# Optimization experiments

Measured on AMD Instinct MI355X. Metric: run time of the kernel, lower is better.

Reference implementation:

```python
import jax, jax.numpy as jnp
import numpy as np

D_MODEL = 1024
NUM_HEADS = 16
D_K = D_MODEL // NUM_HEADS
B, S = 2, 2048


def setup_inputs() -> dict:
    key = jax.random.key(0)
    ks = jax.random.split(key, 11)
    lim = 1.0 / np.sqrt(D_MODEL)  # torch Linear default init range
    def lin(kw, kb):
        W = jax.random.uniform(kw, (D_MODEL, D_MODEL), jnp.float32, -lim, lim)
        b = jax.random.uniform(kb, (D_MODEL,), jnp.float32, -lim, lim)
        return W, b
    Wq, bq = lin(ks[0], ks[1])
    Wk, bk = lin(ks[2], ks[3])
    Wv, bv = lin(ks[4], ks[5])
    Wo, bo = lin(ks[6], ks[7])
    return {
        "Q": jax.random.normal(ks[8], (B, S, D_MODEL), jnp.float32),
        "K": jax.random.normal(ks[9], (B, S, D_MODEL), jnp.float32),
        "V": jax.random.normal(ks[10], (B, S, D_MODEL), jnp.float32),
        "Wq": Wq, "bq": bq, "Wk": Wk, "bk": bk,
        "Wv": Wv, "bv": bv, "Wo": Wo, "bo": bo,
        "validate": False,
    }


def _split_heads(x):
    b, s, _ = x.shape
    return x.reshape(b, s, NUM_HEADS, D_K).transpose(0, 2, 1, 3)  # [B,H,S,Dk]


def reference(Q, K, V, Wq, bq, Wk, bk, Wv, bv, Wo, bo, validate):
    # Linear projections (torch Linear: x @ W.T + b)
    q = _split_heads(Q @ Wq.T + bq)
    k = _split_heads(K @ Wk.T + bk)
    v = _split_heads(V @ Wv.T + bv)
    scale = 1.0 / jnp.sqrt(jnp.asarray(D_K, q.dtype))
    scores = jnp.einsum("bhqd,bhkd->bhqk", q, k) * scale  # [B,H,S,S]
    attn = jax.nn.softmax(scores, axis=-1)
    out = jnp.einsum("bhqk,bhkd->bhqd", attn, v)  # [B,H,S,Dk]
    out = out.transpose(0, 2, 1, 3).reshape(Q.shape[0], Q.shape[1], D_MODEL)
    return out @ Wo.T + bo
```

## Files before the change

kernel.cpp:

```cpp
#include <hip/hip_runtime.h>


typedef short bf16x8 __attribute__((ext_vector_type(8)));
typedef float f32x4 __attribute__((ext_vector_type(4)));

#define D_MODEL 1024
#define NHEAD 16
#define DK 64
#define BB 2
#define SS 2048
#define MROWS (BB * SS)
#define C1 0.18033688011112042f

__device__ __forceinline__ unsigned short f2bf(float f) {
  unsigned u = __builtin_bit_cast(unsigned, f);
  u += 0x7fffu + ((u >> 16) & 1u);
  return (unsigned short)(u >> 16);
}
__device__ __forceinline__ unsigned pack2(float a, float b) {
  return (unsigned)f2bf(a) | ((unsigned)f2bf(b) << 16);
}
__device__ __forceinline__ unsigned cvtpk(float lo, float hi) {
  unsigned r;
  asm("v_cvt_pk_bf16_f32 %0, %1, %2" : "=v"(r) : "v"(lo), "v"(hi));
  return r;
}
__device__ __forceinline__ float max3f(float a, float b, float c) {
  float d;
  asm("v_max3_f32 %0, %1, %2, %3" : "=v"(d) : "v"(a), "v"(b), "v"(c));
  return d;
}

typedef __attribute__((address_space(3))) unsigned int as3u;
typedef const __attribute__((address_space(1))) unsigned int as1u;
__device__ __forceinline__ void gload16(void* lds, const void* g) {
  __builtin_amdgcn_global_load_lds((as1u*)g, (as3u*)lds, 16, 0, 0);
}

struct CvtArgs {
  const float* s[7];
  unsigned short* d[7];
  int n8[7];
};

__global__ __launch_bounds__(256) void convert_bf16(CvtArgs a) {
  const int slot = blockIdx.y;
  const float* __restrict__ s = a.s[slot];
  unsigned short* __restrict__ d = a.d[slot];
  const int n8 = a.n8[slot];
  for (int i = blockIdx.x * 256 + threadIdx.x; i < n8; i += gridDim.x * 256) {
    const size_t off = (size_t)i * 8;
    const float4 v0 = *(const float4*)&s[off];
    const float4 v1 = *(const float4*)&s[off + 4];
    uint4 p;
    p.x = pack2(v0.x, v0.y); p.y = pack2(v0.z, v0.w);
    p.z = pack2(v1.x, v1.y); p.w = pack2(v1.z, v1.w);
    *(uint4*)&d[off] = p;
  }
}

template <int BM, int BN, int MODE>
__device__ __forceinline__ void gemm_core(unsigned short* smem,
                                          const unsigned short* __restrict__ A,
                                          const unsigned short* __restrict__ B,
                                          const float* __restrict__ bias,
                                          float scale, float* __restrict__ Cf,
                                          unsigned short* __restrict__ Cb) {
  const int LDSZ = (BM + BN) * 32;
  const int tid = threadIdx.x;
  const int lane = tid & 63, w = tid >> 6;
  const int wm = w >> 1, wn = w & 1;
  const int l15 = lane & 15, l4 = lane >> 4;
  const int bm = blockIdx.y, bn = blockIdx.x;
  const int MF = BM / 32, NF = BN / 32;

  auto stage = [&](unsigned short* dst, int k0) {
    unsigned short* Asb = dst;
    unsigned short* Bsb = dst + BM * 32;
#pragma unroll
    for (int i = 0; i < BM / 64; ++i) {
      const int flat = i * 256 + tid;
      const int row = flat >> 2, gl = flat & 3;
      const int gs = (gl ^ ((row >> 1) & 3)) * 8;
      gload16(&Asb[flat * 8], &A[(size_t)(bm * BM + row) * D_MODEL + k0 + gs]);
    }
#pragma unroll
    for (int i = 0; i < BN / 64; ++i) {
      const int flat = i * 256 + tid;
      const int row = flat >> 2, gl = flat & 3;
      const int gs = (gl ^ ((row >> 1) & 3)) * 8;
      gload16(&Bsb[flat * 8], &B[(size_t)(bn * BN + row) * D_MODEL + k0 + gs]);
    }
  };

  f32x4 acc[MF][NF];
#pragma unroll
  for (int m = 0; m < MF; ++m)
#pragma unroll
    for (int n = 0; n < NF; ++n) acc[m][n] = (f32x4){0.f, 0.f, 0.f, 0.f};

  stage(smem, 0);
  __syncthreads();
  int cur = 0;
  for (int k0 = 0; k0 < D_MODEL; k0 += 32) {
    if (k0 + 32 < D_MODEL) stage(smem + (cur ^ 1) * LDSZ, k0 + 32);
    unsigned short* As = smem + cur * LDSZ;
    unsigned short* Bs = As + BM * 32;
    bf16x8 af[MF], bf[NF];
#pragma unroll
    for (int m = 0; m < MF; ++m) {
      const int r = wm * (BM / 2) + m * 16 + l15;
      af[m] = *(const bf16x8*)&As[r * 32 + ((((r >> 1) & 3) ^ l4) << 3)];
    }
#pragma unroll
    for (int n = 0; n < NF; ++n) {
      const int r = wn * (BN / 2) + n * 16 + l15;
      bf[n] = *(const bf16x8*)&Bs[r * 32 + ((((r >> 1) & 3) ^ l4) << 3)];
    }
#pragma unroll
    for (int m = 0; m < MF; ++m)
#pragma unroll
      for (int n = 0; n < NF; ++n)
        acc[m][n] = __builtin_amdgcn_mfma_f32_16x16x32_bf16(af[m], bf[n], acc[m][n], 0, 0, 0);
    __syncthreads();
    cur ^= 1;
  }

  if (MODE != 2) {
#pragma unroll
    for (int m = 0; m < MF; ++m)
#pragma unroll
      for (int n = 0; n < NF; ++n) {
        const int col = bn * BN + wn * (BN / 2) + n * 16 + l15;
        const float bv = bias[col];
#pragma unroll
        for (int r = 0; r < 4; ++r) {
          const int row = bm * BM + wm * (BM / 2) + m * 16 + l4 * 4 + r;
          const float v = (acc[m][n][r] + bv) * scale;
          if (MODE == 0) Cb[(size_t)row * D_MODEL + col] = f2bf(v);
          else           Cf[(size_t)row * D_MODEL + col] = v;
        }
      }
  } else {
    unsigned short* T = smem;
#pragma unroll
    for (int m = 0; m < MF; ++m)
#pragma unroll
      for (int n = 0; n < NF; ++n) {
        const int cl = wn * (BN / 2) + n * 16 + l15;
        const float bv = bias[bn * BN + cl];
#pragma unroll
        for (int r = 0; r < 4; ++r) {
          const int rl = wm * (BM / 2) + m * 16 + l4 * 4 + r;
          const int byte = cl * (BM * 2) + ((((rl >> 3) ^ (cl & 7))) << 4) + ((rl & 7) << 1);
          *(unsigned short*)((char*)T + byte) = f2bf(acc[m][n][r] + bv);
        }
      }
    __syncthreads();
#pragma unroll
    for (int c = 0; c < BN * BM / 8 / 256; ++c) {
      const int chunk = c * 256 + tid;
      const int cl = chunk >> 3, rl0 = (chunk & 7) * 8;
      const int byte = cl * (BM * 2) + (((rl0 >> 3) ^ (cl & 7)) << 4);
      const uint4 val = *(const uint4*)((const char*)T + byte);
      const int gcol = bn * BN + cl;
      const int bb = (bm * BM) >> 11;
      const int s = ((bm * BM) & 2047) + rl0;
      *(uint4*)&Cb[(size_t)(bb * 1024 + gcol) * SS + s] = val;
    }
  }
}

__global__ __launch_bounds__(256, 6) void gemm_qkv(
    const unsigned short* __restrict__ Xq, const unsigned short* __restrict__ Xk,
    const unsigned short* __restrict__ Xv,
    const unsigned short* __restrict__ Wq, const float* __restrict__ bq,
    const unsigned short* __restrict__ Wk, const float* __restrict__ bk,
    const unsigned short* __restrict__ Wv, const float* __restrict__ bv,
    unsigned short* __restrict__ q, unsigned short* __restrict__ k,
    unsigned short* __restrict__ vT) {
  __shared__ __align__(16) unsigned short smem[2 * (64 + 128) * 32];
  const int z = blockIdx.z;
  if (z == 0) {
    gemm_core<64, 128, 0>(smem, Xq, Wq, bq, C1, nullptr, q);
  } else if (z == 1) {
    gemm_core<64, 128, 0>(smem, Xk, Wk, bk, 1.0f, nullptr, k);
  } else {
    gemm_core<64, 128, 2>(smem, Xv, Wv, bv, 1.0f, nullptr, vT);
  }
}

__global__ __launch_bounds__(256, 4) void gemm_o(const unsigned short* __restrict__ A,
                                                 const unsigned short* __restrict__ W,
                                                 const float* __restrict__ bi,
                                                 float* __restrict__ out) {
  __shared__ __align__(16) unsigned short smem[2 * (64 + 64) * 32];
  gemm_core<64, 64, 1>(smem, A, W, bi, 1.0f, out, nullptr);
}

__global__ __launch_bounds__(256, 2) void attn_kernel(
    const unsigned short* __restrict__ Qp, const unsigned short* __restrict__ Kp,
    const unsigned short* __restrict__ vTp, unsigned short* __restrict__ Op) {
  __shared__ __align__(16) unsigned short Kt[2][64 * 64];
  __shared__ __align__(16) unsigned short Vt[2][64 * 64];
  __shared__ __align__(16) unsigned short Pt[4][32 * 64];
  const int tid = threadIdx.x;
  const int lane = tid & 63, w = tid >> 6;
  const int l15 = lane & 15, l4 = lane >> 4;
  const int bh = blockIdx.x;
  const int b = bh >> 4, h = bh & 15;
  const int qb = blockIdx.y;
  const size_t baseQ = (size_t)b * SS * D_MODEL + (size_t)h * DK;
  const size_t baseV = (size_t)(b * 1024 + h * 64) * SS;

  bf16x8 aq[2][2];
#pragma unroll
  for (int m = 0; m < 2; ++m) {
    const int qrow = qb * 128 + w * 32 + m * 16 + l15;
#pragma unroll
    for (int kk = 0; kk < 2; ++kk)
      aq[m][kk] = *(const bf16x8*)&Qp[baseQ + (size_t)qrow * D_MODEL + kk * 32 + l4 * 8];
  }

  const bf16x8 vone = {0x3F80, 0x3F80, 0x3F80, 0x3F80, 0x3F80, 0x3F80, 0x3F80, 0x3F80};

  float rm[2] = {-1e30f, -1e30f};
  f32x4 acc[2][5];
#pragma unroll
  for (int m = 0; m < 2; ++m)
#pragma unroll
    for (int d = 0; d < 5; ++d) acc[m][d] = (f32x4){0.f, 0.f, 0.f, 0.f};

  auto stage = [&](int buf, int kt) {
#pragma unroll
    for (int i = 0; i < 2; ++i) {
      const int flat = (w * 2 + i) * 64 + lane;
      const int row = flat >> 3, g = flat & 7;
      gload16(&Kt[buf][flat * 8],
              &Kp[baseQ + (size_t)(kt * 64 + row) * D_MODEL + ((g ^ (row & 7)) << 3)]);
    }
#pragma unroll
    for (int i = 0; i < 2; ++i) {
      const int flat = (w * 2 + i) * 64 + lane;
      const int row = flat >> 3, g = flat & 7;
      gload16(&Vt[buf][flat * 8],
              &vTp[baseV + (size_t)row * SS + kt * 64 + ((g ^ (row & 7)) << 3)]);
    }
  };

  stage(0, 0);
  __syncthreads();
  int cur = 0;
  for (int kt = 0; kt < SS / 64; ++kt) {
    if (kt + 1 < SS / 64) stage(cur ^ 1, kt + 1);

    f32x4 st[2][4];
#pragma unroll
    for (int m = 0; m < 2; ++m)
#pragma unroll
      for (int n = 0; n < 4; ++n) st[m][n] = (f32x4){0.f, 0.f, 0.f, 0.f};
#pragma unroll
    for (int kk = 0; kk < 2; ++kk) {
      bf16x8 kf[4];
#pragma unroll
      for (int n = 0; n < 4; ++n) {
        const int r = n * 16 + l15;
        kf[n] = *(const bf16x8*)&Kt[cur][r * 64 + (((kk * 4 + l4) ^ (r & 7)) << 3)];
      }
#pragma unroll
      for (int m = 0; m < 2; ++m)
#pragma unroll
        for (int n = 0; n < 4; ++n)
          st[m][n] = __builtin_amdgcn_mfma_f32_16x16x32_bf16(kf[n], aq[m][kk], st[m][n], 0, 0, 0);
    }

    float mx[2];
#pragma unroll
    for (int m = 0; m < 2; ++m) {
      const float a0 = max3f(st[m][0][0], st[m][0][1], st[m][0][2]);
      const float a1 = max3f(st[m][0][3], st[m][1][0], st[m][1][1]);
      const float a2 = max3f(st[m][1][2], st[m][1][3], st[m][2][0]);
      const float a3 = max3f(st[m][2][1], st[m][2][2], st[m][2][3]);
      const float a4 = max3f(st[m][3][0], st[m][3][1], st[m][3][2]);
      float v = fmaxf(max3f(a0, a1, a2), max3f(a3, a4, st[m][3][3]));
      v = fmaxf(v, __shfl_xor(v, 16));
      v = fmaxf(v, __shfl_xor(v, 32));
      mx[m] = v;
    }
    if (__any((mx[0] > rm[0] + 8.f) | (mx[1] > rm[1] + 8.f))) {
#pragma unroll
      for (int m = 0; m < 2; ++m) {
        const float nm = fmaxf(rm[m], mx[m]);
        const float alpha = exp2f(rm[m] - nm);
        rm[m] = nm;
#pragma unroll
        for (int r = 0; r < 4; ++r) {
          const float ar = __shfl(alpha, l4 * 4 + r);
#pragma unroll
          for (int d = 0; d < 5; ++d) acc[m][d][r] *= ar;
        }
      }
    }
#pragma unroll
    for (int m = 0; m < 2; ++m)
#pragma unroll
      for (int n = 0; n < 4; ++n)
#pragma unroll
        for (int r = 0; r < 4; ++r) st[m][n][r] = exp2f(st[m][n][r] - rm[m]);

#pragma unroll
    for (int m = 0; m < 2; ++m)
#pragma unroll
      for (int n = 0; n < 4; ++n)
#pragma unroll
        for (int c = 0; c < 2; ++c) {
          const int col = n * 16 + l4 * 4 + 2 * c;
          const int row = m * 16 + l15;
          const int sw = (((col >> 3) ^ (row & 7)) << 3) + (col & 7);
          *(unsigned*)&Pt[w][row * 64 + sw] = cvtpk(st[m][n][2 * c], st[m][n][2 * c + 1]);
        }

#pragma unroll
    for (int kk = 0; kk < 2; ++kk) {
      bf16x8 ap[2], vf[4];
#pragma unroll
      for (int m = 0; m < 2; ++m) {
        const int r = m * 16 + l15;
        ap[m] = *(const bf16x8*)&Pt[w][r * 64 + (((kk * 4 + l4) ^ (r & 7)) << 3)];
      }
#pragma unroll
      for (int d = 0; d < 4; ++d) {
        const int r = d * 16 + l15;
        vf[d] = *(const bf16x8*)&Vt[cur][r * 64 + (((kk * 4 + l4) ^ (r & 7)) << 3)];
      }
#pragma unroll
      for (int m = 0; m < 2; ++m) {
#pragma unroll
        for (int d = 0; d < 4; ++d)
          acc[m][d] = __builtin_amdgcn_mfma_f32_16x16x32_bf16(ap[m], vf[d], acc[m][d], 0, 0, 0);
        acc[m][4] = __builtin_amdgcn_mfma_f32_16x16x32_bf16(ap[m], vone, acc[m][4], 0, 0, 0);
      }
    }

    __syncthreads();
    cur ^= 1;
  }

#pragma unroll
  for (int m = 0; m < 2; ++m) {
    float inv[4];
#pragma unroll
    for (int r = 0; r < 4; ++r) inv[r] = 1.0f / acc[m][4][r];
#pragma unroll
    for (int d = 0; d < 4; ++d)
#pragma unroll
      for (int r = 0; r < 4; ++r) {
        const int orow = qb * 128 + w * 32 + m * 16 + l4 * 4 + r;
        Op[baseQ + (size_t)orow * D_MODEL + d * 16 + l15] = f2bf(acc[m][d][r] * inv[r]);
      }
  }
}

extern "C" void kernel_launch(void* const* d_in, const int* in_sizes, int n_in,
                              void* d_out, int out_size, void* d_ws, size_t ws_size,
                              hipStream_t stream) {
  const float* Qin = (const float*)d_in[0];
  const float* Kin = (const float*)d_in[1];
  const float* Vin = (const float*)d_in[2];
  const float* Wq = (const float*)d_in[3];
  const float* bq = (const float*)d_in[4];
  const float* Wk = (const float*)d_in[5];
  const float* bk = (const float*)d_in[6];
  const float* Wv = (const float*)d_in[7];
  const float* bv = (const float*)d_in[8];
  const float* Wo = (const float*)d_in[9];
  const float* bo = (const float*)d_in[10];
  float* out = (float*)d_out;

  const size_t NX = (size_t)MROWS * D_MODEL;
  const size_t NW = (size_t)D_MODEL * D_MODEL;
  unsigned short* ws = (unsigned short*)d_ws;
  unsigned short* q  = ws;
  unsigned short* k  = ws + NX;
  unsigned short* vT = ws + 2 * NX;
  unsigned short* Xq = ws + 3 * NX;
  unsigned short* Xk = ws + 4 * NX;
  unsigned short* Xv = ws + 5 * NX;
  unsigned short* wq = ws + 6 * NX;
  unsigned short* wk = wq + NW;
  unsigned short* wv = wk + NW;
  unsigned short* wo = wv + NW;
  unsigned short* ao = Xq;

  CvtArgs ca;
  ca.s[0] = Qin; ca.d[0] = Xq; ca.n8[0] = (int)(NX / 8);
  ca.s[1] = Kin; ca.d[1] = Xk; ca.n8[1] = (int)(NX / 8);
  ca.s[2] = Vin; ca.d[2] = Xv; ca.n8[2] = (int)(NX / 8);
  ca.s[3] = Wq;  ca.d[3] = wq; ca.n8[3] = (int)(NW / 8);
  ca.s[4] = Wk;  ca.d[4] = wk; ca.n8[4] = (int)(NW / 8);
  ca.s[5] = Wv;  ca.d[5] = wv; ca.n8[5] = (int)(NW / 8);
  ca.s[6] = Wo;  ca.d[6] = wo; ca.n8[6] = (int)(NW / 8);
  convert_bf16<<<dim3(1024, 7), 256, 0, stream>>>(ca);

  gemm_qkv<<<dim3(D_MODEL / 128, MROWS / 64, 3), 256, 0, stream>>>(
      Xq, Xk, Xv, wq, bq, wk, bk, wv, bv, q, k, vT);
  attn_kernel<<<dim3(BB * NHEAD, SS / 128), 256, 0, stream>>>(q, k, vT, ao);
  gemm_o<<<dim3(D_MODEL / 64, MROWS / 64), 256, 0, stream>>>(ao, wo, bo, out);
}
```

Before: 252.8 us.

## Switch projection GEMMs to 128x128 single-buffered tiles and prioritize MFMA in attention

Replaces the double-buffered 64xN, K=32 GEMM core with a 128x128 tile, K=64 step, single-buffered GEMM used by both the QKV and output projections. The larger tile raises arithmetic intensity per LDS load and halves the barrier count per K. The cost is losing load/compute overlap, and the output GEMM drops to 256 blocks, which may underfill the GPU. Attention MFMA sections are also wrapped in s_setprio to favor matrix issue.

```diff
diff --git a/kernel.cpp b/kernel.cpp
--- a/kernel.cpp
+++ b/kernel.cpp
@@ -59,83 +59,75 @@
   }
 }
 
-template <int BM, int BN, int MODE>
-__device__ __forceinline__ void gemm_core(unsigned short* smem,
-                                          const unsigned short* __restrict__ A,
-                                          const unsigned short* __restrict__ B,
-                                          const float* __restrict__ bias,
-                                          float scale, float* __restrict__ Cf,
-                                          unsigned short* __restrict__ Cb) {
-  const int LDSZ = (BM + BN) * 32;
+template <int MODE>
+__device__ __forceinline__ void gemm128(unsigned short* smem,
+                                        const unsigned short* __restrict__ A,
+                                        const unsigned short* __restrict__ B,
+                                        const float* __restrict__ bias,
+                                        float scale, int bm, int nb,
+                                        float* __restrict__ Cf,
+                                        unsigned short* __restrict__ Cb) {
+  unsigned short* As = smem;
+  unsigned short* Bs = smem + 128 * 64;
   const int tid = threadIdx.x;
   const int lane = tid & 63, w = tid >> 6;
   const int wm = w >> 1, wn = w & 1;
   const int l15 = lane & 15, l4 = lane >> 4;
-  const int bm = blockIdx.y, bn = blockIdx.x;
-  const int MF = BM / 32, NF = BN / 32;
-
-  auto stage = [&](unsigned short* dst, int k0) {
-    unsigned short* Asb = dst;
-    unsigned short* Bsb = dst + BM * 32;
-#pragma unroll
-    for (int i = 0; i < BM / 64; ++i) {
+
+  f32x4 acc[4][4];
+#pragma unroll
+  for (int m = 0; m < 4; ++m)
+#pragma unroll
+    for (int n = 0; n < 4; ++n) acc[m][n] = (f32x4){0.f, 0.f, 0.f, 0.f};
+
+  for (int k0 = 0; k0 < D_MODEL; k0 += 64) {
+    __syncthreads();
+#pragma unroll
+    for (int i = 0; i < 4; ++i) {
       const int flat = i * 256 + tid;
-      const int row = flat >> 2, gl = flat & 3;
-      const int gs = (gl ^ ((row >> 1) & 3)) * 8;
-      gload16(&Asb[flat * 8], &A[(size_t)(bm * BM + row) * D_MODEL + k0 + gs]);
-    }
-#pragma unroll
-    for (int i = 0; i < BN / 64; ++i) {
+      const int row = flat >> 3, g = flat & 7;
+      const int gs = (g ^ (row & 7)) << 3;
+      gload16(&As[flat * 8], &A[(size_t)(bm * 128 + row) * D_MODEL + k0 + gs]);
+    }
+#pragma unroll
+    for (int i = 0; i < 4; ++i) {
       const int flat = i * 256 + tid;
-      const int row = flat >> 2, gl = flat & 3;
-      const int gs = (gl ^ ((row >> 1) & 3)) * 8;
-      gload16(&Bsb[flat * 8], &B[(size_t)(bn * BN + row) * D_MODEL + k0 + gs]);
-    }
-  };
-
-  f32x4 acc[MF][NF];
-#pragma unroll
-  for (int m = 0; m < MF; ++m)
-#pragma unroll
-    for (int n = 0; n < NF; ++n) acc[m][n] = (f32x4){0.f, 0.f, 0.f, 0.f};
-
-  stage(smem, 0);
-  __syncthreads();
-  int cur = 0;
-  for (int k0 = 0; k0 < D_MODEL; k0 += 32) {
-    if (k0 + 32 < D_MODEL) stage(smem + (cur ^ 1) * LDSZ, k0 + 32);
-    unsigned short* As = smem + cur * LDSZ;
-    unsigned short* Bs = As + BM * 32;
-    bf16x8 af[MF], bf[NF];
-#pragma unroll
-    for (int m = 0; m < MF; ++m) {
-      const int r = wm * (BM / 2) + m * 16 + l15;
-      af[m] = *(const bf16x8*)&As[r * 32 + ((((r >> 1) & 3) ^ l4) << 3)];
-    }
-#pragma unroll
-    for (int n = 0; n < NF; ++n) {
-      const int r = wn * (BN / 2) + n * 16 + l15;
-      bf[n] = *(const bf16x8*)&Bs[r * 32 + ((((r >> 1) & 3) ^ l4) << 3)];
-    }
-#pragma unroll
-    for (int m = 0; m < MF; ++m)
-#pragma unroll
-      for (int n = 0; n < NF; ++n)
-        acc[m][n] = __builtin_amdgcn_mfma_f32_16x16x32_bf16(af[m], bf[n], acc[m][n], 0, 0, 0);
+      const int row = flat >> 3, g = flat & 7;
+      const int gs = (g ^ (row & 7)) << 3;
+      gload16(&Bs[flat * 8], &B[(size_t)(nb * 128 + row) * D_MODEL + k0 + gs]);
+    }
     __syncthreads();
-    cur ^= 1;
+#pragma unroll
+    for (int kk = 0; kk < 2; ++kk) {
+      bf16x8 af[4], bf[4];
+#pragma unroll
+      for (int m = 0; m < 4; ++m) {
+        const int r = wm * 64 + m * 16 + l15;
+        af[m] = *(const bf16x8*)&As[r * 64 + (((kk * 4 + l4) ^ (r & 7)) << 3)];
+      }
+#pragma unroll
+      for (int n = 0; n < 4; ++n) {
+        const int r = wn * 64 + n * 16 + l15;
+        bf[n] = *(const bf16x8*)&Bs[r * 64 + (((kk * 4 + l4) ^ (r & 7)) << 3)];
+      }
+#pragma unroll
+      for (int m = 0; m < 4; ++m)
+#pragma unroll
+        for (int n = 0; n < 4; ++n)
+          acc[m][n] = __builtin_amdgcn_mfma_f32_16x16x32_bf16(af[m], bf[n], acc[m][n], 0, 0, 0);
+    }
   }
 
   if (MODE != 2) {
 #pragma unroll
-    for (int m = 0; m < MF; ++m)
-#pragma unroll
-      for (int n = 0; n < NF; ++n) {
-        const int col = bn * BN + wn * (BN / 2) + n * 16 + l15;
+    for (int m = 0; m < 4; ++m)
+#pragma unroll
+      for (int n = 0; n < 4; ++n) {
+        const int col = nb * 128 + wn * 64 + n * 16 + l15;
         const float bv = bias[col];
 #pragma unroll
         for (int r = 0; r < 4; ++r) {
-          const int row = bm * BM + wm * (BM / 2) + m * 16 + l4 * 4 + r;
+          const int row = bm * 128 + wm * 64 + m * 16 + l4 * 4 + r;
           const float v = (acc[m][n][r] + bv) * scale;
           if (MODE == 0) Cb[(size_t)row * D_MODEL + col] = f2bf(v);
           else           Cf[(size_t)row * D_MODEL + col] = v;
@@ -143,35 +135,36 @@
       }
   } else {
     unsigned short* T = smem;
-#pragma unroll
-    for (int m = 0; m < MF; ++m)
-#pragma unroll
-      for (int n = 0; n < NF; ++n) {
-        const int cl = wn * (BN / 2) + n * 16 + l15;
-        const float bv = bias[bn * BN + cl];
+    __syncthreads();
+#pragma unroll
+    for (int m = 0; m < 4; ++m)
+#pragma unroll
+      for (int n = 0; n < 4; ++n) {
+        const int cl = wn * 64 + n * 16 + l15;
+        const float bv = bias[nb * 128 + cl];
 #pragma unroll
         for (int r = 0; r < 4; ++r) {
-          const int rl = wm * (BM / 2) + m * 16 + l4 * 4 + r;
-          const int byte = cl * (BM * 2) + ((((rl >> 3) ^ (cl & 7))) << 4) + ((rl & 7) << 1);
+          const int rl = wm * 64 + m * 16 + l4 * 4 + r;
+          const int byte = cl * 256 + ((((rl >> 3) ^ (cl & 7))) << 4) + ((rl & 7) << 1);
           *(unsigned short*)((char*)T + byte) = f2bf(acc[m][n][r] + bv);
         }
       }
     __syncthreads();
 #pragma unroll
-    for (int c = 0; c < BN * BM / 8 / 256; ++c) {
+    for (int c = 0; c < 8; ++c) {
       const int chunk = c * 256 + tid;
-      const int cl = chunk >> 3, rl0 = (chunk & 7) * 8;
-      const int byte = cl * (BM * 2) + (((rl0 >> 3) ^ (cl & 7)) << 4);
+      const int cl = chunk >> 4, rl0 = (chunk & 15) * 8;
+      const int byte = cl * 256 + (((rl0 >> 3) ^ (cl & 7)) << 4);
       const uint4 val = *(const uint4*)((const char*)T + byte);
-      const int gcol = bn * BN + cl;
-      const int bb = (bm * BM) >> 11;
-      const int s = ((bm * BM) & 2047) + rl0;
+      const int gcol = nb * 128 + cl;
+      const int bb = (bm * 128) >> 11;
+      const int s = ((bm * 128) & 2047) + rl0;
       *(uint4*)&Cb[(size_t)(bb * 1024 + gcol) * SS + s] = val;
     }
   }
 }
 
-__global__ __launch_bounds__(256, 6) void gemm_qkv(
+__global__ __launch_bounds__(256, 3) void gemm_qkv(
     const unsigned short* __restrict__ Xq, const unsigned short* __restrict__ Xk,
     const unsigned short* __restrict__ Xv,
     const unsigned short* __restrict__ Wq, const float* __restrict__ bq,
@@ -179,23 +172,24 @@
     const unsigned short* __restrict__ Wv, const float* __restrict__ bv,
     unsigned short* __restrict__ q, unsigned short* __restrict__ k,
     unsigned short* __restrict__ vT) {
-  __shared__ __align__(16) unsigned short smem[2 * (64 + 128) * 32];
-  const int z = blockIdx.z;
+  __shared__ __align__(16) unsigned short smem[2 * 128 * 64];
+  const int bn = blockIdx.x, bm = blockIdx.y;
+  const int z = bn >> 3, nb = bn & 7;
   if (z == 0) {
-    gemm_core<64, 128, 0>(smem, Xq, Wq, bq, C1, nullptr, q);
+    gemm128<0>(smem, Xq, Wq, bq, C1, bm, nb, nullptr, q);
   } else if (z == 1) {
-    gemm_core<64, 128, 0>(smem, Xk, Wk, bk, 1.0f, nullptr, k);
+    gemm128<0>(smem, Xk, Wk, bk, 1.0f, bm, nb, nullptr, k);
   } else {
-    gemm_core<64, 128, 2>(smem, Xv, Wv, bv, 1.0f, nullptr, vT);
-  }
-}
-
-__global__ __launch_bounds__(256, 4) void gemm_o(const unsigned short* __restrict__ A,
+    gemm128<2>(smem, Xv, Wv, bv, 1.0f, bm, nb, nullptr, vT);
+  }
+}
+
+__global__ __launch_bounds__(256, 3) void gemm_o(const unsigned short* __restrict__ A,
                                                  const unsigned short* __restrict__ W,
                                                  const float* __restrict__ bi,
                                                  float* __restrict__ out) {
-  __shared__ __align__(16) unsigned short smem[2 * (64 + 64) * 32];
-  gemm_core<64, 64, 1>(smem, A, W, bi, 1.0f, out, nullptr);
+  __shared__ __align__(16) unsigned short smem[2 * 128 * 64];
+  gemm128<1>(smem, A, W, bi, 1.0f, blockIdx.y, blockIdx.x, out, nullptr);
 }
 
 __global__ __launch_bounds__(256, 2) void attn_kernel(
@@ -267,11 +261,13 @@
         const int r = n * 16 + l15;
         kf[n] = *(const bf16x8*)&Kt[cur][r * 64 + (((kk * 4 + l4) ^ (r & 7)) << 3)];
       }
+      __builtin_amdgcn_s_setprio(1);
 #pragma unroll
       for (int m = 0; m < 2; ++m)
 #pragma unroll
         for (int n = 0; n < 4; ++n)
           st[m][n] = __builtin_amdgcn_mfma_f32_16x16x32_bf16(kf[n], aq[m][kk], st[m][n], 0, 0, 0);
+      __builtin_amdgcn_s_setprio(0);
     }
 
     float mx[2];
@@ -333,6 +329,7 @@
         const int r = d * 16 + l15;
         vf[d] = *(const bf16x8*)&Vt[cur][r * 64 + (((kk * 4 + l4) ^ (r & 7)) << 3)];
       }
+      __builtin_amdgcn_s_setprio(1);
 #pragma unroll
       for (int m = 0; m < 2; ++m) {
 #pragma unroll
@@ -340,6 +337,7 @@
           acc[m][d] = __builtin_amdgcn_mfma_f32_16x16x32_bf16(ap[m], vf[d], acc[m][d], 0, 0, 0);
         acc[m][4] = __builtin_amdgcn_mfma_f32_16x16x32_bf16(ap[m], vone, acc[m][4], 0, 0, 0);
       }
+      __builtin_amdgcn_s_setprio(0);
     }
 
     __syncthreads();
@@ -402,8 +400,8 @@
   ca.s[6] = Wo;  ca.d[6] = wo; ca.n8[6] = (int)(NW / 8);
   convert_bf16<<<dim3(1024, 7), 256, 0, stream>>>(ca);
 
-  gemm_qkv<<<dim3(D_MODEL / 128, MROWS / 64, 3), 256, 0, stream>>>(
+  gemm_qkv<<<dim3(24, 32), 256, 0, stream>>>(
       Xq, Xk, Xv, wq, bq, wk, bk, wv, bv, q, k, vT);
   attn_kernel<<<dim3(BB * NHEAD, SS / 128), 256, 0, stream>>>(q, k, vT, ao);
-  gemm_o<<<dim3(D_MODEL / 64, MROWS / 64), 256, 0, stream>>>(ao, wo, bo, out);
-}
+  gemm_o<<<dim3(8, 32), 256, 0, stream>>>(ao, wo, bo, out);
+}
```

After: 249.9 us. About the same (-1.2%).
